# Performance work log

Measured on AMD Instinct MI355X. Metric: run time of the kernel, lower is better.

## Reference

```python
import jax, jax.numpy as jnp
import numpy as np
import math

B, S, H, NH = 1, 2048, 1024, 16  # batch, seq, hidden, heads


def setup_inputs() -> dict:
    key = jax.random.key(0)
    ks = jax.random.split(key, 12)
    inp = {
        "query": jax.random.normal(ks[0], (B, S, H), dtype=jnp.float32),
        "key": jax.random.normal(ks[1], (B, S, H), dtype=jnp.float32),
        "value": jax.random.normal(ks[2], (B, S, H), dtype=jnp.float32),
        "attention_mask": jax.random.randint(ks[3], (1, 1, S, S), 0, 2, dtype=jnp.int32),
        # torch nn.Linear params: y = x @ W.T + b, W init ~ U(-1/sqrt(H), 1/sqrt(H))
        "Wq": jax.random.uniform(ks[4], (H, H), jnp.float32, -1, 1) / math.sqrt(H),
        "bq": jax.random.uniform(ks[5], (H,), jnp.float32, -1, 1) / math.sqrt(H),
        "Wk": jax.random.uniform(ks[6], (H, H), jnp.float32, -1, 1) / math.sqrt(H),
        "bk": jax.random.uniform(ks[7], (H,), jnp.float32, -1, 1) / math.sqrt(H),
        "Wv": jax.random.uniform(ks[8], (H, H), jnp.float32, -1, 1) / math.sqrt(H),
        "bv": jax.random.uniform(ks[9], (H,), jnp.float32, -1, 1) / math.sqrt(H),
        "Wo": jax.random.uniform(ks[10], (H, H), jnp.float32, -1, 1) / math.sqrt(H),
        "bo": jax.random.uniform(ks[11], (H,), jnp.float32, -1, 1) / math.sqrt(H),
        "head": NH,
        "hidden_size": H,
    }
    return inp


def reference(query, key, value, attention_mask, Wq, bq, Wk, bk, Wv, bv, Wo, bo, head, hidden_size):
    b, s, _ = query.shape
    d_k = hidden_size // head

    def proj(x, W, bias):
        # [b, s, hidden] -> [b, head, s, d_k]
        y = x @ W.T + bias
        return y.reshape(b, s, head, d_k).transpose(0, 2, 1, 3)

    q = proj(query, Wq, bq)
    k = proj(key, Wk, bk)
    v = proj(value, Wv, bv)

    # naive full score matrix, as in the source (scale by sqrt(d_k) = last dim of q)
    scores = jnp.einsum("bhqd,bhkd->bhqk", q, k) / math.sqrt(d_k)
    # faithful quirk: masked positions are set to 0 (not -inf) before softmax
    scores = jnp.where(attention_mask == 0, jnp.zeros((), scores.dtype), scores)
    attn = jax.nn.softmax(scores, axis=-1)

    out = jnp.einsum("bhqk,bhkd->bhqd", attn, v)  # [b, head, s, d_k]
    out = out.transpose(0, 2, 1, 3).reshape(b, s, head * d_k)
    return out @ Wo.T + bo
```

## Files before the change

kernel.cpp:

```cpp
#include <hip/hip_runtime.h>
#include <hip/hip_bf16.h>


#define S_LEN 2048
#define HID   1024
#define NHEAD 16
#define DK    64

typedef unsigned short u16;
typedef __attribute__((ext_vector_type(8))) short bf16x8;
typedef __attribute__((ext_vector_type(4))) short bf16x4;
typedef __attribute__((ext_vector_type(4))) float f32x4;

__device__ __forceinline__ void load16_lds(const void* g, void* l) {
  __builtin_amdgcn_global_load_lds(
      (const __attribute__((address_space(1))) void*)g,
      (__attribute__((address_space(3))) void*)l, 16, 0, 0);
}

__device__ __forceinline__ short bfbits(float x) {
  __hip_bfloat16 h = __float2bfloat16(x);
  return *(short*)&h;
}
__device__ __forceinline__ bf16x8 cvt8(float4 a, float4 b) {
  bf16x8 r;
  r[0] = bfbits(a.x); r[1] = bfbits(a.y); r[2] = bfbits(a.z); r[3] = bfbits(a.w);
  r[4] = bfbits(b.x); r[5] = bfbits(b.y); r[6] = bfbits(b.z); r[7] = bfbits(b.w);
  return r;
}
__device__ __forceinline__ float bf2f(u16 u) {
  unsigned v = (unsigned)u << 16;
  return *(float*)&v;
}

__global__ __launch_bounds__(256) void cvt_kernel(
    const float* __restrict__ q, const float* __restrict__ k,
    const float* __restrict__ v, const float* __restrict__ wq,
    const float* __restrict__ wk, const float* __restrict__ wv,
    const float* __restrict__ wo, u16* __restrict__ Xbf,
    u16* __restrict__ Wbf) {
  const int y = blockIdx.y;
  size_t i = ((size_t)blockIdx.x * 256 + threadIdx.x) * 8;
  const float* src;
  u16* dst;
  size_t n;
  if (y < 3) {
    src = y == 0 ? q : (y == 1 ? k : v);
    dst = Xbf + (size_t)y * (S_LEN * HID);
    n = (size_t)S_LEN * HID;
  } else {
    int w = y - 3;
    src = w == 0 ? wq : (w == 1 ? wk : (w == 2 ? wv : wo));
    dst = Wbf + (size_t)w * (HID * HID);
    n = (size_t)HID * HID;
  }
  if (i >= n) return;
  float4 a = *(const float4*)(src + i);
  float4 b = *(const float4*)(src + i + 4);
  *(bf16x8*)(dst + i) = cvt8(a, b);
}

__global__ void pack_mask_kernel(const int* __restrict__ mask,
                                 unsigned int* __restrict__ bits) {
  int w = blockIdx.x * blockDim.x + threadIdx.x;
  const int4* p = (const int4*)(mask + (size_t)w * 32);
  unsigned word = 0;
#pragma unroll
  for (int i = 0; i < 8; ++i) {
    int4 v = p[i];
    word |= (unsigned)(v.x != 0) << (i * 4 + 0);
    word |= (unsigned)(v.y != 0) << (i * 4 + 1);
    word |= (unsigned)(v.z != 0) << (i * 4 + 2);
    word |= (unsigned)(v.w != 0) << (i * 4 + 3);
  }
  bits[w] = word;
}

__global__ __launch_bounds__(256) void gemm_qkv(
    const u16* __restrict__ Xbf, const u16* __restrict__ Wbf,
    const float* __restrict__ bq, const float* __restrict__ bk,
    const float* __restrict__ bv, u16* __restrict__ Qb,
    u16* __restrict__ Kb, u16* __restrict__ Vt) {
  constexpr int Mm = 2048, Nn = 1024, Kk = 1024, NIT = 16;
  const int z = blockIdx.z;
  const u16* A = Xbf + (size_t)z * (S_LEN * HID);
  const u16* W = Wbf + (size_t)z * (HID * HID);
  const float* bias = z == 0 ? bq : (z == 1 ? bk : bv);
  u16* C = z == 0 ? Qb : (z == 1 ? Kb : Vt);
  const float oscale = (z == 0) ? 0.125f : 1.0f;
  const int transpose = (z == 2);

  const int tid = threadIdx.x, lane = tid & 63, wave = tid >> 6;
  const int q4 = lane >> 4, c16 = lane & 15;
  const int bx = blockIdx.x;
  const int mBase = (bx & 31) * 64;
  const int nBase = (bx >> 5) * 128;
  const int wn = wave * 32;

  __shared__ __align__(16) u16 As[2][2][64 * 32];
  __shared__ __align__(16) u16 Bs[2][2][128 * 32];

  f32x4 acc[4][2] = {};
  const int srow = lane >> 2, se8 = (lane & 3) * 8;

  auto issue = [&](int it, int buf) {
#pragma unroll
    for (int j = 0; j < 2; ++j) {
      int u = wave * 2 + j, h = u >> 2, grp = u & 3;
      load16_lds(A + (size_t)(mBase + grp * 16 + srow) * Kk + it * 64 +
                     h * 32 + se8,
                 &As[buf][h][grp * 512]);
    }
#pragma unroll
    for (int j = 0; j < 4; ++j) {
      int u = wave * 4 + j, h = u >> 3, grp = u & 7;
      load16_lds(W + (size_t)(nBase + grp * 16 + srow) * Kk + it * 64 +
                     h * 32 + se8,
                 &Bs[buf][h][grp * 512]);
    }
  };

  issue(0, 0);
  __syncthreads();

  for (int it = 0; it < NIT; ++it) {
    const int buf = it & 1, nbuf = buf ^ 1;
    if (it + 1 < NIT) issue(it + 1, nbuf);
#pragma unroll
    for (int kk = 0; kk < 2; ++kk) {
      bf16x8 af[4], bfr[2];
#pragma unroll
      for (int t = 0; t < 4; ++t)
        af[t] = *(const bf16x8*)&As[buf][kk][(t * 16 + c16) * 32 + q4 * 8];
#pragma unroll
      for (int t = 0; t < 2; ++t)
        bfr[t] = *(const bf16x8*)&Bs[buf][kk][(wn + t * 16 + c16) * 32 + q4 * 8];
#pragma unroll
      for (int mt = 0; mt < 4; ++mt)
#pragma unroll
        for (int nt = 0; nt < 2; ++nt)
          acc[mt][nt] = __builtin_amdgcn_mfma_f32_16x16x32_bf16(
              af[mt], bfr[nt], acc[mt][nt], 0, 0, 0);
    }
    __syncthreads();
  }

#pragma unroll
  for (int nt = 0; nt < 2; ++nt) {
    int col = nBase + wn + nt * 16 + c16;
    float bv2 = bias[col];
#pragma unroll
    for (int mt = 0; mt < 4; ++mt) {
#pragma unroll
      for (int r = 0; r < 4; ++r) {
        int row = mBase + mt * 16 + q4 * 4 + r;
        float v = (acc[mt][nt][r] + bv2) * oscale;
        if (transpose)
          ((__hip_bfloat16*)C)[(size_t)col * Mm + row] = __float2bfloat16(v);
        else
          ((__hip_bfloat16*)C)[(size_t)row * Nn + col] = __float2bfloat16(v);
      }
    }
  }
}

__global__ __launch_bounds__(512) void attn_kernel(
    const u16* __restrict__ Qb, const u16* __restrict__ Kb,
    const u16* __restrict__ Vt, const unsigned* __restrict__ mbits,
    u16* __restrict__ partO, float* __restrict__ partL) {
  constexpr int NITA = S_LEN / 2 / 64;
  const int qt = blockIdx.x, h = blockIdx.y, zz = blockIdx.z;
  const int tid = threadIdx.x, lane = tid & 63, wave = tid >> 6;
  const int q4 = lane >> 4, c16 = lane & 15;

  __shared__ __align__(16) u16 Ks[2][2][64 * 32];
  __shared__ __align__(16) u16 Vs[2][2][64 * 32];
  __shared__ __align__(16) u16 Ps[8][16 * 72];

  const int wq0 = qt * 128 + wave * 16;

  bf16x8 qf[2];
#pragma unroll
  for (int kk = 0; kk < 2; ++kk)
    qf[kk] = *(const bf16x8*)(Qb + (size_t)(wq0 + c16) * HID + h * DK +
                              kk * 32 + q4 * 8);

  f32x4 o[4] = {};
  float l_lane[4] = {};

  const int srow = lane >> 2;
  const int se8  = (lane & 3) * 8;
  const int kvbase = zz * (S_LEN / 2);

  auto issueKV = [&](int it, int buf) {
    const int kv0 = kvbase + it * 64;
#pragma unroll
    for (int j = 0; j < 2; ++j) {
      int i = wave * 2 + j;
      if (i < 8) {
        int half = i >> 2, grp = i & 3;
        load16_lds(Kb + (size_t)(kv0 + grp * 16 + srow) * HID + h * DK +
                       half * 32 + se8,
                   &Ks[buf][half][grp * 512]);
      } else {
        int ii = i - 8;
        int half = ii >> 2, grp = ii & 3;
        load16_lds(Vt + (size_t)(h * DK + grp * 16 + srow) * S_LEN + kv0 +
                       half * 32 + se8,
                   &Vs[buf][half][grp * 512]);
      }
    }
  };

  issueKV(0, 0);
  __syncthreads();

  for (int it = 0; it < NITA; ++it) {
    const int buf = it & 1, nbuf = buf ^ 1;
    const int kv0 = kvbase + it * 64;
    if (it + 1 < NITA) issueKV(it + 1, nbuf);

    f32x4 sv[4];
#pragma unroll
    for (int nt = 0; nt < 4; ++nt) {
      bf16x8 kf0 = *(const bf16x8*)&Ks[buf][0][(nt * 16 + c16) * 32 + q4 * 8];
      bf16x8 kf1 = *(const bf16x8*)&Ks[buf][1][(nt * 16 + c16) * 32 + q4 * 8];
      f32x4 a = {};
      a = __builtin_amdgcn_mfma_f32_16x16x32_bf16(qf[0], kf0, a, 0, 0, 0);
      a = __builtin_amdgcn_mfma_f32_16x16x32_bf16(qf[1], kf1, a, 0, 0, 0);
      sv[nt] = a;
    }

#pragma unroll
    for (int r = 0; r < 4; ++r) {
      int row = wq0 + q4 * 4 + r;
      const unsigned* mrow = mbits + (size_t)row * 64 + (kv0 >> 5);
      unsigned w0 = mrow[0], w1 = mrow[1];
#pragma unroll
      for (int nt = 0; nt < 4; ++nt) {
        unsigned word = (nt < 2) ? w0 : w1;
        int bit = ((nt & 1) * 16) + c16;
        float s = ((word >> bit) & 1u) ? sv[nt][r] : 0.0f;
        float p = __expf(s);
        sv[nt][r] = p;
        l_lane[r] += p;
      }
    }

    u16* pw = &Ps[wave][0];
#pragma unroll
    for (int r = 0; r < 4; ++r)
#pragma unroll
      for (int nt = 0; nt < 4; ++nt)
        ((__hip_bfloat16*)pw)[(q4 * 4 + r) * 72 + nt * 16 + c16] =
            __float2bfloat16(sv[nt][r]);
    asm volatile("s_waitcnt lgkmcnt(0)" ::: "memory");

#pragma unroll
    for (int kk = 0; kk < 2; ++kk) {
      bf16x8 pa = *(const bf16x8*)&pw[c16 * 72 + kk * 32 + q4 * 8];
#pragma unroll
      for (int nt = 0; nt < 4; ++nt) {
        bf16x8 vb = *(const bf16x8*)&Vs[buf][kk][(nt * 16 + c16) * 32 + q4 * 8];
        o[nt] = __builtin_amdgcn_mfma_f32_16x16x32_bf16(pa, vb, o[nt], 0, 0, 0);
      }
    }
    __syncthreads();
  }

#pragma unroll
  for (int r = 0; r < 4; ++r) {
    float s = l_lane[r];
#pragma unroll
    for (int d = 1; d < 16; d <<= 1) s += __shfl_xor(s, d);
    l_lane[r] = s;
  }

#pragma unroll
  for (int r = 0; r < 4; ++r) {
    int row = wq0 + q4 * 4 + r;
#pragma unroll
    for (int nt = 0; nt < 4; ++nt)
      ((__hip_bfloat16*)partO)[((size_t)zz * S_LEN + row) * HID + h * DK +
                               nt * 16 + c16] = __float2bfloat16(o[nt][r]);
    if (c16 == 0)
      partL[((size_t)zz * NHEAD + h) * S_LEN + row] = l_lane[r];
  }
}

__global__ __launch_bounds__(256) void combine_kernel(
    const u16* __restrict__ partO, const float* __restrict__ partL,
    u16* __restrict__ ctx) {
  size_t idx = ((size_t)blockIdx.x * 256 + threadIdx.x) * 4;
  int row = (int)(idx >> 10);
  int col = (int)(idx & 1023);
  int h = col >> 6;
  float l = partL[(size_t)h * S_LEN + row] +
            partL[((size_t)NHEAD + h) * S_LEN + row];
  float inv = 1.0f / l;
  bf16x4 a = *(const bf16x4*)(partO + idx);
  bf16x4 b = *(const bf16x4*)(partO + (size_t)S_LEN * HID + idx);
  bf16x4 r;
#pragma unroll
  for (int j = 0; j < 4; ++j) {
    float v = (bf2f((u16)a[j]) + bf2f((u16)b[j])) * inv;
    r[j] = bfbits(v);
  }
  *(bf16x4*)(ctx + idx) = r;
}

__global__ __launch_bounds__(256) void gemm_out(
    const u16* __restrict__ ctx, const u16* __restrict__ Wo,
    const float* __restrict__ bo, float* __restrict__ out) {
  constexpr int Nn = 1024, Kk = 1024, NIT = 16;
  const int tid = threadIdx.x, lane = tid & 63, wave = tid >> 6;
  const int q4 = lane >> 4, c16 = lane & 15;
  const int bx = blockIdx.x;
  const int mBase = (bx & 63) * 32;
  const int nBase = (bx >> 6) * 128;
  const int wn = wave * 32;

  __shared__ __align__(16) u16 As[2][2][32 * 32];
  __shared__ __align__(16) u16 Bs[2][2][128 * 32];

  f32x4 acc[2][2] = {};
  const int srow = lane >> 2, se8 = (lane & 3) * 8;

  auto issue = [&](int it, int buf) {
    {
      int u = wave, h = u >> 1, grp = u & 1;
      load16_lds(ctx + (size_t)(mBase + grp * 16 + srow) * Kk + it * 64 +
                     h * 32 + se8,
                 &As[buf][h][grp * 512]);
    }
#pragma unroll
    for (int j = 0; j < 4; ++j) {
      int u = wave * 4 + j, h = u >> 3, grp = u & 7;
      load16_lds(Wo + (size_t)(nBase + grp * 16 + srow) * Kk + it * 64 +
                     h * 32 + se8,
                 &Bs[buf][h][grp * 512]);
    }
  };

  issue(0, 0);
  __syncthreads();

  for (int it = 0; it < NIT; ++it) {
    const int buf = it & 1, nbuf = buf ^ 1;
    if (it + 1 < NIT) issue(it + 1, nbuf);
#pragma unroll
    for (int kk = 0; kk < 2; ++kk) {
      bf16x8 af[2], bfr[2];
#pragma unroll
      for (int t = 0; t < 2; ++t)
        af[t] = *(const bf16x8*)&As[buf][kk][(t * 16 + c16) * 32 + q4 * 8];
#pragma unroll
      for (int t = 0; t < 2; ++t)
        bfr[t] = *(const bf16x8*)&Bs[buf][kk][(wn + t * 16 + c16) * 32 + q4 * 8];
#pragma unroll
      for (int mt = 0; mt < 2; ++mt)
#pragma unroll
        for (int nt = 0; nt < 2; ++nt)
          acc[mt][nt] = __builtin_amdgcn_mfma_f32_16x16x32_bf16(
              af[mt], bfr[nt], acc[mt][nt], 0, 0, 0);
    }
    __syncthreads();
  }

#pragma unroll
  for (int nt = 0; nt < 2; ++nt) {
    int col = nBase + wn + nt * 16 + c16;
    float bv = bo[col];
#pragma unroll
    for (int mt = 0; mt < 2; ++mt)
#pragma unroll
      for (int r = 0; r < 4; ++r) {
        int row = mBase + mt * 16 + q4 * 4 + r;
        out[(size_t)row * Nn + col] = acc[mt][nt][r] + bv;
      }
  }
}

extern "C" void kernel_launch(void* const* d_in, const int* in_sizes, int n_in,
                              void* d_out, int out_size, void* d_ws, size_t ws_size,
                              hipStream_t stream) {
  const float* q    = (const float*)d_in[0];
  const float* k    = (const float*)d_in[1];
  const float* v    = (const float*)d_in[2];
  const int*   mask = (const int*)d_in[3];
  const float* Wq = (const float*)d_in[4];
  const float* bq = (const float*)d_in[5];
  const float* Wk = (const float*)d_in[6];
  const float* bk = (const float*)d_in[7];
  const float* Wv = (const float*)d_in[8];
  const float* bv = (const float*)d_in[9];
  const float* Wo = (const float*)d_in[10];
  const float* bo = (const float*)d_in[11];

  const size_t M2 = (size_t)S_LEN * HID;
  const size_t W1 = (size_t)HID * HID;
  const size_t need = (4 * W1 + 3 * M2 + 3 * M2) * 2 +
                      (size_t)S_LEN * 64 * 4 + 2 * NHEAD * S_LEN * 4;
  if (ws_size < need) return;

  u16* Wbf = (u16*)d_ws;
  u16* Xbf = Wbf + 4 * W1;
  u16* partO = Xbf;
  u16* Qb = Xbf + 3 * M2;
  u16* Kb = Qb + M2;
  u16* Vt = Kb + M2;
  unsigned* mbits = (unsigned*)(Vt + M2);
  float* partL = (float*)(mbits + (size_t)S_LEN * 64);
  u16* ctx = Qb;

  hipLaunchKernelGGL(cvt_kernel, dim3(1024, 7), dim3(256), 0, stream,
                     q, k, v, Wq, Wk, Wv, Wo, Xbf, Wbf);

  hipLaunchKernelGGL(pack_mask_kernel, dim3((S_LEN * (S_LEN / 32)) / 256),
                     dim3(256), 0, stream, mask, mbits);

  hipLaunchKernelGGL(gemm_qkv, dim3(256, 1, 3), dim3(256), 0, stream,
                     Xbf, Wbf, bq, bk, bv, Qb, Kb, Vt);

  hipLaunchKernelGGL(attn_kernel, dim3(S_LEN / 128, NHEAD, 2), dim3(512), 0,
                     stream, Qb, Kb, Vt, mbits, partO, partL);

  hipLaunchKernelGGL(combine_kernel, dim3((S_LEN * HID / 4) / 256), dim3(256),
                     0, stream, partO, partL, ctx);

  hipLaunchKernelGGL(gemm_out, dim3(512), dim3(256), 0, stream,
                     ctx, Wbf + 3 * W1, bo, (float*)d_out);
}
```

Baseline: 203.4 us.

## Retile attention to 32 query rows per wave with 4-way KV split and swizzled LDS

Each wave now processes 32 query rows instead of 16, reusing every K/V fragment read from LDS for two MFMA row tiles, and the KV sequence is split four ways instead of two. The mask bits are stored transposed so each lane fetches its row words with one vector load, and the log2e factor is folded into the Q scale so exp2f replaces __expf. K/V LDS tiles use an XOR swizzle to cut bank conflicts, and partial outputs are placed in reused workspace, including the Wq/Wk bf16 region, which is no longer needed at that point. The costs are a wider combine step reading four partials, and more registers per wave under a new launch bound.

```diff
diff --git a/kernel.cpp b/kernel.cpp
--- a/kernel.cpp
+++ b/kernel.cpp
@@ -11,6 +11,7 @@
 typedef __attribute__((ext_vector_type(8))) short bf16x8;
 typedef __attribute__((ext_vector_type(4))) short bf16x4;
 typedef __attribute__((ext_vector_type(4))) float f32x4;
+typedef __attribute__((ext_vector_type(4))) unsigned u32x4;
 
 __device__ __forceinline__ void load16_lds(const void* g, void* l) {
   __builtin_amdgcn_global_load_lds(
@@ -60,10 +61,11 @@
   *(bf16x8*)(dst + i) = cvt8(a, b);
 }
 
-__global__ void pack_mask_kernel(const int* __restrict__ mask,
-                                 unsigned int* __restrict__ bits) {
-  int w = blockIdx.x * blockDim.x + threadIdx.x;
-  const int4* p = (const int4*)(mask + (size_t)w * 32);
+__global__ __launch_bounds__(256) void pack_mask_kernel(
+    const int* __restrict__ mask, unsigned int* __restrict__ bitsT) {
+  int idx = blockIdx.x * 256 + threadIdx.x;
+  int row = idx & 2047, widx = idx >> 11;
+  const int4* p = (const int4*)(mask + (size_t)row * S_LEN + widx * 32);
   unsigned word = 0;
 #pragma unroll
   for (int i = 0; i < 8; ++i) {
@@ -73,7 +75,7 @@
     word |= (unsigned)(v.z != 0) << (i * 4 + 2);
     word |= (unsigned)(v.w != 0) << (i * 4 + 3);
   }
-  bits[w] = word;
+  bitsT[(size_t)widx * S_LEN + row] = word;
 }
 
 __global__ __launch_bounds__(256) void gemm_qkv(
@@ -87,7 +89,7 @@
   const u16* W = Wbf + (size_t)z * (HID * HID);
   const float* bias = z == 0 ? bq : (z == 1 ? bk : bv);
   u16* C = z == 0 ? Qb : (z == 1 ? Kb : Vt);
-  const float oscale = (z == 0) ? 0.125f : 1.0f;
+  const float oscale = (z == 0) ? 0.125f * 1.44269504088896f : 1.0f;
   const int transpose = (z == 2);
 
   const int tid = threadIdx.x, lane = tid & 63, wave = tid >> 6;
@@ -164,33 +166,37 @@
   }
 }
 
-__global__ __launch_bounds__(512) void attn_kernel(
+__global__ __launch_bounds__(512, 4) void attn_kernel(
     const u16* __restrict__ Qb, const u16* __restrict__ Kb,
-    const u16* __restrict__ Vt, const unsigned* __restrict__ mbits,
-    u16* __restrict__ partO, float* __restrict__ partL) {
-  constexpr int NITA = S_LEN / 2 / 64;
+    const u16* __restrict__ Vt, const unsigned* __restrict__ mbT,
+    u16* __restrict__ partOA, u16* __restrict__ partO3,
+    float* __restrict__ partL) {
+  constexpr int NITA = 8;
   const int qt = blockIdx.x, h = blockIdx.y, zz = blockIdx.z;
   const int tid = threadIdx.x, lane = tid & 63, wave = tid >> 6;
   const int q4 = lane >> 4, c16 = lane & 15;
 
   __shared__ __align__(16) u16 Ks[2][2][64 * 32];
   __shared__ __align__(16) u16 Vs[2][2][64 * 32];
-  __shared__ __align__(16) u16 Ps[8][16 * 72];
-
-  const int wq0 = qt * 128 + wave * 16;
-
-  bf16x8 qf[2];
-#pragma unroll
-  for (int kk = 0; kk < 2; ++kk)
-    qf[kk] = *(const bf16x8*)(Qb + (size_t)(wq0 + c16) * HID + h * DK +
-                              kk * 32 + q4 * 8);
-
-  f32x4 o[4] = {};
-  float l_lane[4] = {};
+  __shared__ __align__(16) u16 Ps[8][32 * 72];
+
+  const int q0 = qt * 256 + wave * 32;
+
+  bf16x8 qf[2][2];
+#pragma unroll
+  for (int m = 0; m < 2; ++m)
+#pragma unroll
+    for (int kk = 0; kk < 2; ++kk)
+      qf[m][kk] = *(const bf16x8*)(Qb + (size_t)(q0 + m * 16 + c16) * HID +
+                                   h * DK + kk * 32 + q4 * 8);
+
+  f32x4 o[2][4] = {};
+  float l_lane[2][4] = {{}, {}};
+  const unsigned mlo = 1u << c16, mhi = mlo << 16;
 
   const int srow = lane >> 2;
-  const int se8  = (lane & 3) * 8;
-  const int kvbase = zz * (S_LEN / 2);
+  const int sslot = ((lane & 3) ^ (srow & 3)) * 8;
+  const int kvbase = zz * (S_LEN / 4);
 
   auto issueKV = [&](int it, int buf) {
     const int kv0 = kvbase + it * 64;
@@ -200,13 +206,13 @@
       if (i < 8) {
         int half = i >> 2, grp = i & 3;
         load16_lds(Kb + (size_t)(kv0 + grp * 16 + srow) * HID + h * DK +
-                       half * 32 + se8,
+                       half * 32 + sslot,
                    &Ks[buf][half][grp * 512]);
       } else {
         int ii = i - 8;
         int half = ii >> 2, grp = ii & 3;
         load16_lds(Vt + (size_t)(h * DK + grp * 16 + srow) * S_LEN + kv0 +
-                       half * 32 + se8,
+                       half * 32 + sslot,
                    &Vs[buf][half][grp * 512]);
       }
     }
@@ -215,95 +221,98 @@
   issueKV(0, 0);
   __syncthreads();
 
+  __hip_bfloat16* pw = (__hip_bfloat16*)&Ps[wave][0];
+
   for (int it = 0; it < NITA; ++it) {
     const int buf = it & 1, nbuf = buf ^ 1;
-    const int kv0 = kvbase + it * 64;
     if (it + 1 < NITA) issueKV(it + 1, nbuf);
 
-    f32x4 sv[4];
+    const unsigned* mr = mbT + (size_t)(zz * 16 + it * 2) * S_LEN + q0 + q4 * 4;
+    u32x4 mwa[2][2];
+#pragma unroll
+    for (int m = 0; m < 2; ++m) {
+      mwa[m][0] = *(const u32x4*)(mr + m * 16);
+      mwa[m][1] = *(const u32x4*)(mr + S_LEN + m * 16);
+    }
+
 #pragma unroll
     for (int nt = 0; nt < 4; ++nt) {
-      bf16x8 kf0 = *(const bf16x8*)&Ks[buf][0][(nt * 16 + c16) * 32 + q4 * 8];
-      bf16x8 kf1 = *(const bf16x8*)&Ks[buf][1][(nt * 16 + c16) * 32 + q4 * 8];
-      f32x4 a = {};
-      a = __builtin_amdgcn_mfma_f32_16x16x32_bf16(qf[0], kf0, a, 0, 0, 0);
-      a = __builtin_amdgcn_mfma_f32_16x16x32_bf16(qf[1], kf1, a, 0, 0, 0);
-      sv[nt] = a;
-    }
-
+      const int rsw = (nt * 16 + c16) * 32 + ((q4 ^ (c16 & 3)) * 8);
+      bf16x8 kf0 = *(const bf16x8*)&Ks[buf][0][rsw];
+      bf16x8 kf1 = *(const bf16x8*)&Ks[buf][1][rsw];
+#pragma unroll
+      for (int m = 0; m < 2; ++m) {
+        f32x4 a = {};
+        a = __builtin_amdgcn_mfma_f32_16x16x32_bf16(qf[m][0], kf0, a, 0, 0, 0);
+        a = __builtin_amdgcn_mfma_f32_16x16x32_bf16(qf[m][1], kf1, a, 0, 0, 0);
+#pragma unroll
+        for (int r = 0; r < 4; ++r) {
+          unsigned word = mwa[m][nt >> 1][r];
+          unsigned keep = word & ((nt & 1) ? mhi : mlo);
+          float s = keep ? a[r] : 0.0f;
+          float p = exp2f(s);
+          l_lane[m][r] += p;
+          pw[(m * 16 + q4 * 4 + r) * 72 + nt * 16 + c16] = __float2bfloat16(p);
+        }
+      }
+    }
+
+    asm volatile("s_waitcnt lgkmcnt(0)" ::: "memory");
+
+#pragma unroll
+    for (int kk = 0; kk < 2; ++kk) {
+      bf16x8 pa0 = *(const bf16x8*)&Ps[wave][(c16) * 72 + kk * 32 + q4 * 8];
+      bf16x8 pa1 = *(const bf16x8*)&Ps[wave][(16 + c16) * 72 + kk * 32 + q4 * 8];
+#pragma unroll
+      for (int nt = 0; nt < 4; ++nt) {
+        const int rsw = (nt * 16 + c16) * 32 + ((q4 ^ (c16 & 3)) * 8);
+        bf16x8 vb = *(const bf16x8*)&Vs[buf][kk][rsw];
+        o[0][nt] = __builtin_amdgcn_mfma_f32_16x16x32_bf16(pa0, vb, o[0][nt], 0, 0, 0);
+        o[1][nt] = __builtin_amdgcn_mfma_f32_16x16x32_bf16(pa1, vb, o[1][nt], 0, 0, 0);
+      }
+    }
+    __syncthreads();
+  }
+
+  u16* pO = (zz < 3) ? (partOA + (size_t)zz * (S_LEN * HID)) : partO3;
+#pragma unroll
+  for (int m = 0; m < 2; ++m)
 #pragma unroll
     for (int r = 0; r < 4; ++r) {
-      int row = wq0 + q4 * 4 + r;
-      const unsigned* mrow = mbits + (size_t)row * 64 + (kv0 >> 5);
-      unsigned w0 = mrow[0], w1 = mrow[1];
-#pragma unroll
-      for (int nt = 0; nt < 4; ++nt) {
-        unsigned word = (nt < 2) ? w0 : w1;
-        int bit = ((nt & 1) * 16) + c16;
-        float s = ((word >> bit) & 1u) ? sv[nt][r] : 0.0f;
-        float p = __expf(s);
-        sv[nt][r] = p;
-        l_lane[r] += p;
-      }
-    }
-
-    u16* pw = &Ps[wave][0];
-#pragma unroll
-    for (int r = 0; r < 4; ++r)
+      float s = l_lane[m][r];
+#pragma unroll
+      for (int d = 1; d < 16; d <<= 1) s += __shfl_xor(s, d);
+      int row = q0 + m * 16 + q4 * 4 + r;
 #pragma unroll
       for (int nt = 0; nt < 4; ++nt)
-        ((__hip_bfloat16*)pw)[(q4 * 4 + r) * 72 + nt * 16 + c16] =
-            __float2bfloat16(sv[nt][r]);
-    asm volatile("s_waitcnt lgkmcnt(0)" ::: "memory");
-
-#pragma unroll
-    for (int kk = 0; kk < 2; ++kk) {
-      bf16x8 pa = *(const bf16x8*)&pw[c16 * 72 + kk * 32 + q4 * 8];
-#pragma unroll
-      for (int nt = 0; nt < 4; ++nt) {
-        bf16x8 vb = *(const bf16x8*)&Vs[buf][kk][(nt * 16 + c16) * 32 + q4 * 8];
-        o[nt] = __builtin_amdgcn_mfma_f32_16x16x32_bf16(pa, vb, o[nt], 0, 0, 0);
-      }
-    }
-    __syncthreads();
-  }
-
-#pragma unroll
-  for (int r = 0; r < 4; ++r) {
-    float s = l_lane[r];
-#pragma unroll
-    for (int d = 1; d < 16; d <<= 1) s += __shfl_xor(s, d);
-    l_lane[r] = s;
-  }
-
-#pragma unroll
-  for (int r = 0; r < 4; ++r) {
-    int row = wq0 + q4 * 4 + r;
-#pragma unroll
-    for (int nt = 0; nt < 4; ++nt)
-      ((__hip_bfloat16*)partO)[((size_t)zz * S_LEN + row) * HID + h * DK +
-                               nt * 16 + c16] = __float2bfloat16(o[nt][r]);
-    if (c16 == 0)
-      partL[((size_t)zz * NHEAD + h) * S_LEN + row] = l_lane[r];
-  }
+        ((__hip_bfloat16*)pO)[(size_t)row * HID + h * DK + nt * 16 + c16] =
+            __float2bfloat16(o[m][nt][r]);
+      if (c16 == 0)
+        partL[((size_t)zz * NHEAD + h) * S_LEN + row] = s;
+    }
 }
 
 __global__ __launch_bounds__(256) void combine_kernel(
-    const u16* __restrict__ partO, const float* __restrict__ partL,
-    u16* __restrict__ ctx) {
+    const u16* __restrict__ pOA, const u16* __restrict__ pO3,
+    const float* __restrict__ partL, u16* __restrict__ ctx) {
   size_t idx = ((size_t)blockIdx.x * 256 + threadIdx.x) * 4;
   int row = (int)(idx >> 10);
   int col = (int)(idx & 1023);
   int h = col >> 6;
-  float l = partL[(size_t)h * S_LEN + row] +
-            partL[((size_t)NHEAD + h) * S_LEN + row];
+  float l = 0.0f;
+#pragma unroll
+  for (int z = 0; z < 4; ++z)
+    l += partL[((size_t)z * NHEAD + h) * S_LEN + row];
   float inv = 1.0f / l;
-  bf16x4 a = *(const bf16x4*)(partO + idx);
-  bf16x4 b = *(const bf16x4*)(partO + (size_t)S_LEN * HID + idx);
+  bf16x4 a0 = *(const bf16x4*)(pOA + idx);
+  bf16x4 a1 = *(const bf16x4*)(pOA + (size_t)S_LEN * HID + idx);
+  bf16x4 a2 = *(const bf16x4*)(pOA + 2 * (size_t)S_LEN * HID + idx);
+  bf16x4 a3 = *(const bf16x4*)(pO3 + idx);
   bf16x4 r;
 #pragma unroll
   for (int j = 0; j < 4; ++j) {
-    float v = (bf2f((u16)a[j]) + bf2f((u16)b[j])) * inv;
+    float v = (bf2f((u16)a0[j]) + bf2f((u16)a1[j]) + bf2f((u16)a2[j]) +
+               bf2f((u16)a3[j])) * inv;
     r[j] = bfbits(v);
   }
   *(bf16x4*)(ctx + idx) = r;
@@ -405,12 +414,13 @@
 
   u16* Wbf = (u16*)d_ws;
   u16* Xbf = Wbf + 4 * W1;
-  u16* partO = Xbf;
   u16* Qb = Xbf + 3 * M2;
   u16* Kb = Qb + M2;
   u16* Vt = Kb + M2;
   unsigned* mbits = (unsigned*)(Vt + M2);
-  float* partL = (float*)(mbits + (size_t)S_LEN * 64);
+  u16* partOA = Xbf;
+  u16* partO3 = Wbf;
+  float* partL = (float*)(Wbf + 2 * W1);
   u16* ctx = Qb;
 
   hipLaunchKernelGGL(cvt_kernel, dim3(1024, 7), dim3(256), 0, stream,
@@ -422,11 +432,11 @@
   hipLaunchKernelGGL(gemm_qkv, dim3(256, 1, 3), dim3(256), 0, stream,
                      Xbf, Wbf, bq, bk, bv, Qb, Kb, Vt);
 
-  hipLaunchKernelGGL(attn_kernel, dim3(S_LEN / 128, NHEAD, 2), dim3(512), 0,
-                     stream, Qb, Kb, Vt, mbits, partO, partL);
+  hipLaunchKernelGGL(attn_kernel, dim3(S_LEN / 256, NHEAD, 4), dim3(512), 0,
+                     stream, Qb, Kb, Vt, mbits, partOA, partO3, partL);
 
   hipLaunchKernelGGL(combine_kernel, dim3((S_LEN * HID / 4) / 256), dim3(256),
-                     0, stream, partO, partL, ctx);
+                     0, stream, partOA, partO3, partL, ctx);
 
   hipLaunchKernelGGL(gemm_out, dim3(512), dim3(256), 0, stream,
                      ctx, Wbf + 3 * W1, bo, (float*)d_out);
```

Measured after the change: 227.0 us. 1.12x slower.
